# Kernel optimization log

Measured on AMD Instinct MI355X. Metric: run time of the kernel, lower is better.

## Reference

```python
import jax, jax.numpy as jnp
import numpy as np

N, T, CIN, H, L, NC = 64, 150, 150, 1024, 3, 60
EPS = 1e-5


def setup_inputs() -> dict:
    key = jax.random.key(0)
    ks = jax.random.split(key, 12)
    s = 0.05
    return {
        "x": jax.random.normal(ks[0], (N, T, CIN), jnp.float32),
        "bn_gamma": jnp.ones((CIN,), jnp.float32),
        "bn_beta": jnp.zeros((CIN,), jnp.float32),
        "w_ih0": jax.random.normal(ks[1], (2, 3 * H, CIN), jnp.float32) * s,
        "w_hh0": jax.random.normal(ks[2], (2, 3 * H, H), jnp.float32) * s,
        "b_ih0": jax.random.normal(ks[3], (2, 3 * H), jnp.float32) * s,
        "b_hh0": jax.random.normal(ks[4], (2, 3 * H), jnp.float32) * s,
        "w_ih": jax.random.normal(ks[5], (L - 1, 2, 3 * H, 2 * H), jnp.float32) * s,
        "w_hh": jax.random.normal(ks[6], (L - 1, 2, 3 * H, H), jnp.float32) * s,
        "b_ih": jax.random.normal(ks[7], (L - 1, 2, 3 * H), jnp.float32) * s,
        "b_hh": jax.random.normal(ks[8], (L - 1, 2, 3 * H), jnp.float32) * s,
        "fc_w": jax.random.normal(ks[9], (NC, 2 * H), jnp.float32) * s,
        "fc_b": jax.random.normal(ks[10], (NC,), jnp.float32) * s,
    }


def _bigru_layer(x, w_ih, w_hh, b_ih, b_hh):
    # x: [T, N, I]. Faithful to the source's per-timestep loop: BOTH directions
    # scan forward in time (the 'reverse' direction never sees a reversed seq,
    # since the original feeds length-1 slices while carrying hidden state).
    # Precompute input projections for the whole sequence: [T, 2, N, 3H]
    gi = jnp.einsum('tni,dgi->tdng', x, w_ih) + b_ih[None, :, None, :]

    def step(h, gi_t):
        # h: [2, N, H], gi_t: [2, N, 3H]
        gh = jnp.einsum('dnh,dgh->dng', h, w_hh) + b_hh[:, None, :]
        r = jax.nn.sigmoid(gi_t[..., :H] + gh[..., :H])
        z = jax.nn.sigmoid(gi_t[..., H:2 * H] + gh[..., H:2 * H])
        n = jnp.tanh(gi_t[..., 2 * H:] + r * gh[..., 2 * H:])
        h_new = (1.0 - z) * n + z * h
        out = jnp.concatenate([h_new[0], h_new[1]], axis=-1)  # [N, 2H]
        return h_new, out

    h0 = jnp.zeros((2, x.shape[1], H), x.dtype)
    _, outs = jax.lax.scan(step, h0, gi)
    return outs  # [T, N, 2H]


def reference(x, bn_gamma, bn_beta, w_ih0, w_hh0, b_ih0, b_hh0,
              w_ih, w_hh, b_ih, b_hh, fc_w, fc_b):
    # BatchNorm1d over channels, train mode: batch stats over (N, T), biased var.
    mean = x.mean(axis=(0, 1))
    var = x.var(axis=(0, 1))
    xn = (x - mean) * jax.lax.rsqrt(var + EPS) * bn_gamma + bn_beta

    h = jnp.transpose(xn, (1, 0, 2))  # [T, N, CIN]
    h = _bigru_layer(h, w_ih0, w_hh0, b_ih0, b_hh0)
    for l in range(L - 1):  # small fixed layer loop
        h = _bigru_layer(h, w_ih[l], w_hh[l], b_ih[l], b_hh[l])

    # seq_len == T for every sample, so the gathered hidden is the last step.
    last = h[-1]  # [N, 2H]
    return last @ fc_w.T + fc_b  # [N, num_class]
```

## Files before the change

kernel.cpp:

```cpp
#include <hip/hip_runtime.h>
#include <math.h>

#define NB   64
#define TT   150
#define CIN  150
#define HH   1024
#define G3   3072
#define NCOL 6144
#define KP0  160
#define RT   9600
#define NC   60
#define NSLOT 151
#define SLOT_STRIDE 66560

using bf16x8 = __attribute__((ext_vector_type(8))) __bf16;
using f32x4  = __attribute__((ext_vector_type(4))) float;

static __device__ __forceinline__ unsigned short f2bf(float f){
  unsigned int x = __builtin_bit_cast(unsigned int, f);
  x += 0x7fffu + ((x >> 16) & 1u);
  return (unsigned short)(x >> 16);
}
static __device__ __forceinline__ float bf2f(unsigned short u){
  unsigned int x = ((unsigned int)u) << 16;
  return __builtin_bit_cast(float, x);
}
static __device__ __forceinline__ float sigmoidf(float x){
  return 1.0f / (1.0f + expf(-x));
}

static __device__ __forceinline__ void gload16(const void* g, void* l){
  __builtin_amdgcn_global_load_lds(
      (const __attribute__((address_space(1))) void*)g,
      (__attribute__((address_space(3))) void*)l, 16, 0, 0);
}

__global__ void bn_stats(const float* __restrict__ x, const float* __restrict__ gamma,
                         const float* __restrict__ beta, float* __restrict__ ss){
  const int c = blockIdx.x;
  float s = 0.f, s2 = 0.f;
  for (int i = threadIdx.x; i < RT; i += 256){
    float v = x[(size_t)i * CIN + c];
    s += v; s2 += v * v;
  }
  __shared__ float sh1[256], sh2[256];
  sh1[threadIdx.x] = s; sh2[threadIdx.x] = s2;
  __syncthreads();
  for (int st = 128; st > 0; st >>= 1){
    if ((int)threadIdx.x < st){
      sh1[threadIdx.x] += sh1[threadIdx.x + st];
      sh2[threadIdx.x] += sh2[threadIdx.x + st];
    }
    __syncthreads();
  }
  if (threadIdx.x == 0){
    float mean = sh1[0] * (1.f / RT);
    float var  = sh2[0] * (1.f / RT) - mean * mean;
    float sc   = rsqrtf(var + 1e-5f) * gamma[c];
    ss[c]       = sc;
    ss[CIN + c] = beta[c] - mean * sc;
  }
}

__global__ void bn_apply(const float* __restrict__ x, const float* __restrict__ ss,
                         unsigned short* __restrict__ xn){
  int idx = blockIdx.x * 256 + threadIdx.x;
  if (idx >= RT * KP0) return;
  int r = idx / KP0, c = idx - r * KP0;
  int t = r >> 6, n = r & 63;
  float v = 0.f;
  if (c < CIN) v = x[((size_t)n * TT + t) * CIN + c] * ss[c] + ss[CIN + c];
  xn[idx] = f2bf(v);
}

__global__ void cast_bf(const float* __restrict__ s, unsigned short* __restrict__ d, int n){
  for (int i = blockIdx.x * 256 + threadIdx.x; i < n; i += gridDim.x * 256)
    d[i] = f2bf(s[i]);
}

__global__ void cast_pad_w0(const float* __restrict__ w, unsigned short* __restrict__ d){
  int idx = blockIdx.x * 256 + threadIdx.x;
  if (idx >= NCOL * KP0) return;
  int row = idx / KP0, c = idx - row * KP0;
  d[idx] = (c < CIN) ? f2bf(w[(size_t)row * CIN + c]) : (unsigned short)0;
}

__global__ void zero16(uint4* p, int n){
  int i = blockIdx.x * 256 + threadIdx.x;
  if (i < n) p[i] = make_uint4(0u, 0u, 0u, 0u);
}

__global__ void guard_k(float* out){ out[0] = -12345.0f; }

__global__ __launch_bounds__(256) void gemm_tile(
    const unsigned short* __restrict__ A, const unsigned short* __restrict__ B,
    const float* __restrict__ bias, unsigned short* __restrict__ C, int K)
{
  const int r0 = blockIdx.x * 128;
  const int c0 = blockIdx.y * 128;
  const int tid = threadIdx.x;
  const int wid = tid >> 6;
  const int l   = tid & 63;
  const int lr  = l & 15;
  const int lk  = (l >> 4) * 8;
  const int wm  = wid >> 1;
  const int wn  = wid & 1;

  __shared__ unsigned short As[128 * 32];
  __shared__ unsigned short Bs[128 * 32];

  const int c1   = wid * 64 + l;
  const int rowS = c1 >> 2;
  const int ccS  = c1 & 3;

  f32x4 acc[4][4];
#pragma unroll
  for (int i = 0; i < 4; ++i)
#pragma unroll
    for (int j = 0; j < 4; ++j) acc[i][j] = f32x4{0,0,0,0};

  const unsigned short* Ag0 = A + (size_t)(r0 + rowS) * K + ccS * 8;
  const unsigned short* Ag1 = A + (size_t)(r0 + 64 + rowS) * K + ccS * 8;
  const unsigned short* Bg0 = B + (size_t)(c0 + rowS) * K + ccS * 8;
  const unsigned short* Bg1 = B + (size_t)(c0 + 64 + rowS) * K + ccS * 8;
  unsigned short* As0 = As + wid * 512;
  unsigned short* As1 = As + 2048 + wid * 512;
  unsigned short* Bs0 = Bs + wid * 512;
  unsigned short* Bs1 = Bs + 2048 + wid * 512;

  for (int k0 = 0; k0 < K; k0 += 32){
    gload16(Ag0 + k0, As0);
    gload16(Ag1 + k0, As1);
    gload16(Bg0 + k0, Bs0);
    gload16(Bg1 + k0, Bs1);
    __syncthreads();

    bf16x8 af[4], bfr[4];
#pragma unroll
    for (int mt = 0; mt < 4; ++mt)
      af[mt] = *(const bf16x8*)(As + (wm * 64 + mt * 16 + lr) * 32 + lk);
#pragma unroll
    for (int nt = 0; nt < 4; ++nt)
      bfr[nt] = *(const bf16x8*)(Bs + (wn * 64 + nt * 16 + lr) * 32 + lk);
#pragma unroll
    for (int mt = 0; mt < 4; ++mt)
#pragma unroll
      for (int nt = 0; nt < 4; ++nt)
        acc[mt][nt] = __builtin_amdgcn_mfma_f32_16x16x32_bf16(af[mt], bfr[nt], acc[mt][nt], 0, 0, 0);
    __syncthreads();
  }

  const int rb = (l >> 4) * 4;
#pragma unroll
  for (int mt = 0; mt < 4; ++mt){
#pragma unroll
    for (int nt = 0; nt < 4; ++nt){
      const int col = c0 + wn * 64 + nt * 16 + lr;
      const float bv = bias[col];
#pragma unroll
      for (int reg = 0; reg < 4; ++reg){
        const int row = r0 + wm * 64 + mt * 16 + rb + reg;
        C[(size_t)row * NCOL + col] = f2bf(acc[mt][nt][reg] + bv);
      }
    }
  }
}

__global__ __launch_bounds__(256, 1) void gru_layer(
    const unsigned short* __restrict__ whh,
    const float* __restrict__ bhh,
    const unsigned short* __restrict__ gi,
    unsigned short* __restrict__ outb,
    float* __restrict__ hfinal,
    unsigned short* __restrict__ hbig,
    int* __restrict__ flags, int wout)
{
  const int d  = blockIdx.x >> 6;
  const int jt = blockIdx.x & 63;
  const int j0 = jt * 16;
  const int w  = threadIdx.x >> 6;
  const int l  = threadIdx.x & 63;
  const int lr = l & 15;
  const int hi = l >> 4;

  __shared__ unsigned char wlds[98304];

  {
    const unsigned short* wsrc = whh + (size_t)d * (G3 * HH);
    for (int c = threadIdx.x; c < 6144; c += 256){
      int g   = c >> 11;
      int rem = c & 2047;
      int r   = rem >> 7;
      int kc  = rem & 127;
      uint4 v = *(const uint4*)(wsrc + (size_t)(g * HH + j0 + r) * HH + kc * 8);
      int kcs = (kc & ~7) | ((kc + r) & 7);
      *(uint4*)(wlds + g * 32768 + r * 2048 + kcs * 16) = v;
    }
  }
  __syncthreads();

  const float4 br4 = *(const float4*)(bhh + d * G3 +          j0 + hi * 4);
  const float4 bz4 = *(const float4*)(bhh + d * G3 + HH +     j0 + hi * 4);
  const float4 bn4 = *(const float4*)(bhh + d * G3 + 2 * HH + j0 + hi * 4);

  const int n    = w * 16 + lr;
  const int jcol = j0 + hi * 4;

  unsigned short* dirbase = hbig + (size_t)d * NSLOT * SLOT_STRIDE;
  int* ctr = &flags[d * 64];

  float hold[4] = {0.f, 0.f, 0.f, 0.f};

  for (int t = 0; t < TT; ++t){
    const unsigned short* hprev = dirbase + (size_t)t * SLOT_STRIDE;
    unsigned short*       hnext = dirbase + (size_t)(t + 1) * SLOT_STRIDE;

    size_t gbase = (size_t)(t * NB + n) * NCOL + (size_t)d * G3 + jcol;
    ushort4 gr4 = *(const ushort4*)(gi + gbase);
    ushort4 gz4 = *(const ushort4*)(gi + gbase + HH);
    ushort4 gn4 = *(const ushort4*)(gi + gbase + 2 * HH);

    if (t){
      if (threadIdx.x == 0){
        const int tgt = 64 * t;
        int cap = 0;
        while (__hip_atomic_load(ctr, __ATOMIC_RELAXED, __HIP_MEMORY_SCOPE_AGENT) < tgt){
          if (++cap > 20000000) break;
          __builtin_amdgcn_s_sleep(2);
        }
      }
      __syncthreads();
    }

    f32x4 ar = {0,0,0,0}, az = {0,0,0,0}, an = {0,0,0,0};
    const unsigned short* hrow = hprev + (size_t)(w * 16 + lr) * HH + hi * 8;

    bf16x8 ha[8], hb[8];
#pragma unroll
    for (int i = 0; i < 8; ++i) ha[i] = *(const bf16x8*)(hrow + i * 32);

#pragma unroll
    for (int blk = 0; blk < 4; ++blk){
      if (blk < 3){
#pragma unroll
        for (int i = 0; i < 8; ++i)
          hb[i] = *(const bf16x8*)(hrow + (blk + 1) * 256 + i * 32);
      }
#pragma unroll
      for (int i = 0; i < 8; ++i){
        const int k0  = blk * 256 + i * 32;
        const int kc  = (k0 >> 3) + hi;
        const int kcs = (kc & ~7) | ((kc + lr) & 7);
        const int off = lr * 2048 + kcs * 16;
        bf16x8 a_r = *(const bf16x8*)(wlds +          off);
        bf16x8 a_z = *(const bf16x8*)(wlds + 32768 +  off);
        bf16x8 a_n = *(const bf16x8*)(wlds + 65536 +  off);
        ar = __builtin_amdgcn_mfma_f32_16x16x32_bf16(a_r, ha[i], ar, 0, 0, 0);
        az = __builtin_amdgcn_mfma_f32_16x16x32_bf16(a_z, ha[i], az, 0, 0, 0);
        an = __builtin_amdgcn_mfma_f32_16x16x32_bf16(a_n, ha[i], an, 0, 0, 0);
      }
      if (blk < 3){
#pragma unroll
        for (int i = 0; i < 8; ++i) ha[i] = hb[i];
      }
    }

    {
      ushort4 hb_;
      const float* br = (const float*)&br4;
      const float* bz = (const float*)&bz4;
      const float* bn_ = (const float*)&bn4;
      const unsigned short* g_r = (const unsigned short*)&gr4;
      const unsigned short* g_z = (const unsigned short*)&gz4;
      const unsigned short* g_n = (const unsigned short*)&gn4;
#pragma unroll
      for (int reg = 0; reg < 4; ++reg){
        float r  = sigmoidf(bf2f(g_r[reg]) + ar[reg] + br[reg]);
        float z  = sigmoidf(bf2f(g_z[reg]) + az[reg] + bz[reg]);
        float nn = tanhf(bf2f(g_n[reg]) + r * (an[reg] + bn_[reg]));
        hold[reg] = (1.f - z) * nn + z * hold[reg];
      }
      hb_.x = f2bf(hold[0]); hb_.y = f2bf(hold[1]);
      hb_.z = f2bf(hold[2]); hb_.w = f2bf(hold[3]);
      __hip_atomic_store((unsigned long long*)(hnext + (size_t)n * HH + jcol),
                         __builtin_bit_cast(unsigned long long, hb_),
                         __ATOMIC_RELAXED, __HIP_MEMORY_SCOPE_AGENT);
      if (wout)
        *(ushort4*)(outb + (size_t)(t * NB + n) * (2 * HH) + (size_t)d * HH + jcol) = hb_;
      if (t == TT - 1)
        *(float4*)(hfinal + (size_t)(d * NB + n) * HH + jcol) =
            make_float4(hold[0], hold[1], hold[2], hold[3]);
    }

    __syncthreads();
    if (threadIdx.x == 0)
      __hip_atomic_fetch_add(ctr, 1, __ATOMIC_RELEASE, __HIP_MEMORY_SCOPE_AGENT);
  }
}

__global__ void fc_kernel(const float* __restrict__ hf, const float* __restrict__ fw,
                          const float* __restrict__ fb, float* __restrict__ out){
  int b = blockIdx.x;
  int n = b / NC, c = b - n * NC;
  int l = threadIdx.x;
  float s = 0.f;
  for (int k = l; k < 2 * HH; k += 64){
    float hv = (k < HH) ? hf[(size_t)n * HH + k]
                        : hf[(size_t)(NB + n) * HH + (k - HH)];
    s += hv * fw[(size_t)c * (2 * HH) + k];
  }
#pragma unroll
  for (int off = 32; off > 0; off >>= 1) s += __shfl_down(s, off);
  if (l == 0) out[n * NC + c] = s + fb[c];
}

extern "C" void kernel_launch(void* const* d_in, const int* in_sizes, int n_in,
                              void* d_out, int out_size, void* d_ws, size_t ws_size,
                              hipStream_t stream)
{
  const float* x      = (const float*)d_in[0];
  const float* gamma  = (const float*)d_in[1];
  const float* beta   = (const float*)d_in[2];
  const float* w_ih0  = (const float*)d_in[3];
  const float* w_hh0  = (const float*)d_in[4];
  const float* b_ih0  = (const float*)d_in[5];
  const float* b_hh0  = (const float*)d_in[6];
  const float* w_ih   = (const float*)d_in[7];
  const float* w_hh   = (const float*)d_in[8];
  const float* b_ih   = (const float*)d_in[9];
  const float* b_hh   = (const float*)d_in[10];
  const float* fc_w   = (const float*)d_in[11];
  const float* fc_b   = (const float*)d_in[12];
  float* out = (float*)d_out;

  char* ws = (char*)d_ws;
  size_t off = 0;
  auto alloc = [&](size_t bytes)->void*{
    void* p = ws + off; off += (bytes + 255) & ~(size_t)255; return p;
  };
  unsigned short* whh_bf = (unsigned short*)alloc((size_t)3 * 2 * G3 * HH * 2);
  unsigned short* w0_bf  = (unsigned short*)alloc((size_t)NCOL * KP0 * 2);
  unsigned short* wih_bf = (unsigned short*)alloc((size_t)2 * NCOL * 2 * HH * 2);
  unsigned short* xn_bf  = (unsigned short*)alloc((size_t)RT * KP0 * 2);
  unsigned short* gi_bf  = (unsigned short*)alloc((size_t)RT * NCOL * 2);
  unsigned short* out0   = (unsigned short*)alloc((size_t)RT * 2 * HH * 2);
  unsigned short* out1   = (unsigned short*)alloc((size_t)RT * 2 * HH * 2);
  float* hfinal = (float*)alloc((size_t)2 * NB * HH * 4);
  unsigned short* hbig = (unsigned short*)alloc((size_t)2 * NSLOT * SLOT_STRIDE * 2);
  float* ss = (float*)alloc(2048);
  int* flags = (int*)alloc(1024);

  if (off > ws_size){ guard_k<<<1, 1, 0, stream>>>(out); return; }

  bn_stats<<<CIN, 256, 0, stream>>>(x, gamma, beta, ss);
  bn_apply<<<(RT * KP0 + 255) / 256, 256, 0, stream>>>(x, ss, xn_bf);
  cast_pad_w0<<<(NCOL * KP0 + 255) / 256, 256, 0, stream>>>(w_ih0, w0_bf);
  cast_bf<<<4096, 256, 0, stream>>>(w_hh0, whh_bf, 2 * G3 * HH);
  cast_bf<<<4096, 256, 0, stream>>>(w_hh,  whh_bf + (size_t)2 * G3 * HH, 2 * 2 * G3 * HH);
  cast_bf<<<4096, 256, 0, stream>>>(w_ih,  wih_bf, 2 * NCOL * 2 * HH);

  zero16<<<32, 256, 0, stream>>>((uint4*)hbig, NB * HH * 2 / 16);
  zero16<<<32, 256, 0, stream>>>((uint4*)(hbig + (size_t)NSLOT * SLOT_STRIDE),
                                 NB * HH * 2 / 16);

  for (int lyr = 0; lyr < 3; ++lyr){
    if (lyr == 0){
      gemm_tile<<<dim3(RT / 128, NCOL / 128), 256, 0, stream>>>(xn_bf, w0_bf, b_ih0, gi_bf, KP0);
    } else {
      const unsigned short* Ain = (lyr == 1) ? out0 : out1;
      gemm_tile<<<dim3(RT / 128, NCOL / 128), 256, 0, stream>>>(
          Ain, wih_bf + (size_t)(lyr - 1) * NCOL * 2 * HH,
          b_ih + (size_t)(lyr - 1) * NCOL, gi_bf, 2 * HH);
    }
    zero16<<<1, 32, 0, stream>>>((uint4*)flags, 512 / 16);

    const unsigned short* whh_l = whh_bf + (size_t)lyr * 2 * G3 * HH;
    const float* bhh_l = (lyr == 0) ? b_hh0 : (b_hh + (size_t)(lyr - 1) * NCOL);
    unsigned short* outb = (lyr == 0) ? out0 : out1;
    int wout = (lyr < 2) ? 1 : 0;
    gru_layer<<<128, 256, 0, stream>>>(whh_l, bhh_l, gi_bf, outb,
                                       hfinal, hbig, flags, wout);
  }
  fc_kernel<<<NB * NC, 64, 0, stream>>>(hfinal, fc_w, fc_b, out);
}
```

Baseline: 6.390 ms.

## Split GRU recurrent K dimension across two wave groups with LDS reduction

The persistent GRU recurrence kernel now launches 512 threads per block instead of 256, and splits the hidden-size K reduction in half across two groups of four waves. The second group writes its partial MFMA accumulators into shared memory, and the first group adds them before applying the gate math. This is meant to shorten the serial per-timestep critical path by doubling the MFMA/LDS parallelism per block. The cost is an extra barrier and an LDS reduction each step. The spin-wait sleep interval is also shortened to cut polling latency.

```diff
diff --git a/kernel.cpp b/kernel.cpp
--- a/kernel.cpp
+++ b/kernel.cpp
@@ -166,7 +166,7 @@
   }
 }
 
-__global__ __launch_bounds__(256, 1) void gru_layer(
+__global__ __launch_bounds__(512, 1) void gru_layer(
     const unsigned short* __restrict__ whh,
     const float* __restrict__ bhh,
     const unsigned short* __restrict__ gi,
@@ -178,16 +178,20 @@
   const int d  = blockIdx.x >> 6;
   const int jt = blockIdx.x & 63;
   const int j0 = jt * 16;
-  const int w  = threadIdx.x >> 6;
-  const int l  = threadIdx.x & 63;
+  const int tid = threadIdx.x;
+  const int w  = tid >> 6;
+  const int wq = w & 3;
+  const int kh = w >> 2;
+  const int l  = tid & 63;
   const int lr = l & 15;
   const int hi = l >> 4;
 
   __shared__ unsigned char wlds[98304];
+  __shared__ f32x4 red[3][256];
 
   {
     const unsigned short* wsrc = whh + (size_t)d * (G3 * HH);
-    for (int c = threadIdx.x; c < 6144; c += 256){
+    for (int c = tid; c < 6144; c += 512){
       int g   = c >> 11;
       int rem = c & 2047;
       int r   = rem >> 7;
@@ -199,11 +203,14 @@
   }
   __syncthreads();
 
-  const float4 br4 = *(const float4*)(bhh + d * G3 +          j0 + hi * 4);
-  const float4 bz4 = *(const float4*)(bhh + d * G3 + HH +     j0 + hi * 4);
-  const float4 bn4 = *(const float4*)(bhh + d * G3 + 2 * HH + j0 + hi * 4);
-
-  const int n    = w * 16 + lr;
+  float4 br4 = make_float4(0, 0, 0, 0), bz4 = br4, bn4 = br4;
+  if (w < 4){
+    br4 = *(const float4*)(bhh + d * G3 +          j0 + hi * 4);
+    bz4 = *(const float4*)(bhh + d * G3 + HH +     j0 + hi * 4);
+    bn4 = *(const float4*)(bhh + d * G3 + 2 * HH + j0 + hi * 4);
+  }
+
+  const int n    = wq * 16 + lr;
   const int jcol = j0 + hi * 4;
 
   unsigned short* dirbase = hbig + (size_t)d * NSLOT * SLOT_STRIDE;
@@ -215,41 +222,44 @@
     const unsigned short* hprev = dirbase + (size_t)t * SLOT_STRIDE;
     unsigned short*       hnext = dirbase + (size_t)(t + 1) * SLOT_STRIDE;
 
-    size_t gbase = (size_t)(t * NB + n) * NCOL + (size_t)d * G3 + jcol;
-    ushort4 gr4 = *(const ushort4*)(gi + gbase);
-    ushort4 gz4 = *(const ushort4*)(gi + gbase + HH);
-    ushort4 gn4 = *(const ushort4*)(gi + gbase + 2 * HH);
+    ushort4 gr4, gz4, gn4;
+    if (w < 4){
+      size_t gbase = (size_t)(t * NB + n) * NCOL + (size_t)d * G3 + jcol;
+      gr4 = *(const ushort4*)(gi + gbase);
+      gz4 = *(const ushort4*)(gi + gbase + HH);
+      gn4 = *(const ushort4*)(gi + gbase + 2 * HH);
+    }
 
     if (t){
-      if (threadIdx.x == 0){
+      if (tid == 0){
         const int tgt = 64 * t;
         int cap = 0;
         while (__hip_atomic_load(ctr, __ATOMIC_RELAXED, __HIP_MEMORY_SCOPE_AGENT) < tgt){
           if (++cap > 20000000) break;
-          __builtin_amdgcn_s_sleep(2);
+          __builtin_amdgcn_s_sleep(1);
         }
       }
       __syncthreads();
     }
 
     f32x4 ar = {0,0,0,0}, az = {0,0,0,0}, an = {0,0,0,0};
-    const unsigned short* hrow = hprev + (size_t)(w * 16 + lr) * HH + hi * 8;
-
-    bf16x8 ha[8], hb[8];
+    const unsigned short* hrow = hprev + (size_t)n * HH + kh * 512 + hi * 8;
+
+    bf16x8 ha[8], hb2[8];
 #pragma unroll
     for (int i = 0; i < 8; ++i) ha[i] = *(const bf16x8*)(hrow + i * 32);
 
 #pragma unroll
-    for (int blk = 0; blk < 4; ++blk){
-      if (blk < 3){
+    for (int half = 0; half < 2; ++half){
+      if (half == 0){
 #pragma unroll
         for (int i = 0; i < 8; ++i)
-          hb[i] = *(const bf16x8*)(hrow + (blk + 1) * 256 + i * 32);
+          hb2[i] = *(const bf16x8*)(hrow + 256 + i * 32);
       }
 #pragma unroll
       for (int i = 0; i < 8; ++i){
-        const int k0  = blk * 256 + i * 32;
-        const int kc  = (k0 >> 3) + hi;
+        const int it  = half * 8 + i;
+        const int kc  = kh * 64 + it * 4 + hi;
         const int kcs = (kc & ~7) | ((kc + lr) & 7);
         const int off = lr * 2048 + kcs * 16;
         bf16x8 a_r = *(const bf16x8*)(wlds +          off);
@@ -259,13 +269,25 @@
         az = __builtin_amdgcn_mfma_f32_16x16x32_bf16(a_z, ha[i], az, 0, 0, 0);
         an = __builtin_amdgcn_mfma_f32_16x16x32_bf16(a_n, ha[i], an, 0, 0, 0);
       }
-      if (blk < 3){
-#pragma unroll
-        for (int i = 0; i < 8; ++i) ha[i] = hb[i];
-      }
-    }
-
-    {
+      if (half == 0){
+#pragma unroll
+        for (int i = 0; i < 8; ++i) ha[i] = hb2[i];
+      }
+    }
+
+    __syncthreads();
+    if (w >= 4){
+      red[0][wq * 64 + l] = ar;
+      red[1][wq * 64 + l] = az;
+      red[2][wq * 64 + l] = an;
+    }
+    __syncthreads();
+
+    if (w < 4){
+      ar += red[0][wq * 64 + l];
+      az += red[1][wq * 64 + l];
+      an += red[2][wq * 64 + l];
+
       ushort4 hb_;
       const float* br = (const float*)&br4;
       const float* bz = (const float*)&bz4;
@@ -293,7 +315,7 @@
     }
 
     __syncthreads();
-    if (threadIdx.x == 0)
+    if (tid == 0)
       __hip_atomic_fetch_add(ctr, 1, __ATOMIC_RELEASE, __HIP_MEMORY_SCOPE_AGENT);
   }
 }
@@ -378,7 +400,7 @@
     const float* bhh_l = (lyr == 0) ? b_hh0 : (b_hh + (size_t)(lyr - 1) * NCOL);
     unsigned short* outb = (lyr == 0) ? out0 : out1;
     int wout = (lyr < 2) ? 1 : 0;
-    gru_layer<<<128, 256, 0, stream>>>(whh_l, bhh_l, gi_bf, outb,
+    gru_layer<<<128, 512, 0, stream>>>(whh_l, bhh_l, gi_bf, outb,
                                        hfinal, hbig, flags, wout);
   }
   fc_kernel<<<NB * NC, 64, 0, stream>>>(hfinal, fc_w, fc_b, out);
```

After: 5.444 ms (median of 2 runs). 1.17x faster.
